# Optimization experiments

Hardware: AMD Instinct MI355X
Metric: run time of the kernel (lower is better)

## Reference

```python
import jax, jax.numpy as jnp
import numpy as np

B = 65536      # batch
D = 512        # embedding_dim
H = 256        # hidden_size
NB = 6         # num_branch


def setup_inputs() -> dict:
    key = jax.random.key(0)
    ks = jax.random.split(key, 12)
    sc = 0.05
    s = lambda k, shape: (jax.random.normal(k, shape, jnp.float32) * sc)
    inp = {}
    inp["embedding"] = jax.random.normal(ks[0], (B, D), jnp.float32)
    inp["speed"] = jax.random.normal(ks[1], (B,), jnp.float32)
    inp["command"] = jax.random.randint(ks[2], (B,), 1, NB + 1)  # values 1..6
    # speed_in: Linear(1,H) -> ReLU -> Linear(H,D)   (weights stored [in,out])
    inp["sw1"] = s(ks[3], (1, H)); inp["sb1"] = jnp.zeros((H,), jnp.float32)
    inp["sw2"] = s(ks[4], (H, D)); inp["sb2"] = jnp.zeros((D,), jnp.float32)
    # 6 branch MLPs, stacked along leading axis: D->H->H->3, sigmoid
    inp["bw1"] = s(ks[5], (NB, D, H)); inp["bb1"] = jnp.zeros((NB, H), jnp.float32)
    inp["bw2"] = s(ks[6], (NB, H, H)); inp["bb2"] = jnp.zeros((NB, H), jnp.float32)
    inp["bw3"] = s(ks[7], (NB, H, 3)); inp["bb3"] = jnp.zeros((NB, 3), jnp.float32)
    # speed_out: D->H->H->1
    inp["ow1"] = s(ks[8], (D, H)); inp["ob1"] = jnp.zeros((H,), jnp.float32)
    inp["ow2"] = s(ks[9], (H, H)); inp["ob2"] = jnp.zeros((H,), jnp.float32)
    inp["ow3"] = s(ks[10], (H, 1)); inp["ob3"] = jnp.zeros((1,), jnp.float32)
    return inp


def reference(embedding, speed, command,
              sw1, sb1, sw2, sb2,
              bw1, bb1, bw2, bb2, bw3, bb3,
              ow1, ob1, ow2, ob2, ow3, ob3):
    # embedding += speed_in(speed.unsqueeze(1))
    sh = jax.nn.relu(speed[:, None] @ sw1 + sb1)           # [B,H]
    emb = embedding + (sh @ sw2 + sb2)                      # [B,D]

    # all 6 branches computed densely (as in the original), then masked
    h = jax.nn.relu(jnp.einsum('bd,ndh->nbh', emb, bw1) + bb1[:, None, :])   # [NB,B,H]
    h = jax.nn.relu(jnp.einsum('nbh,nhk->nbk', h, bw2) + bb2[:, None, :])    # [NB,B,H]
    br = jax.nn.sigmoid(jnp.einsum('nbh,nho->nbo', h, bw3) + bb3[:, None, :])  # [NB,B,3]

    # mask: branch i selected where i == command - 1
    mask = (jnp.arange(NB)[:, None] == (command - 1)[None, :]).astype(br.dtype)  # [NB,B]
    control_pred = jnp.sum(br * mask[:, :, None], axis=0)   # [B,3]

    # speed_out head
    t = jax.nn.relu(emb @ ow1 + ob1)
    t = jax.nn.relu(t @ ow2 + ob2)
    speed_pred = t @ ow3 + ob3                               # [B,1]
    return control_pred, speed_pred
```

## Files before the change

kernel.cpp:

```cpp
#include <hip/hip_runtime.h>
#include <math.h>


#define B_ 65536
#define D_ 512
#define H_ 256

typedef float  f32x4   __attribute__((ext_vector_type(4)));
typedef __bf16 bf16x8  __attribute__((ext_vector_type(8)));
typedef __bf16 bf16x4  __attribute__((ext_vector_type(4)));
typedef float  float4v __attribute__((ext_vector_type(4)));

#define OFF_CURSORS  64
#define OFF_PERM     256
#define OFF_PACK     262400
#define WS_NEEDED    3277056

#define PKO_SW2   0u
#define PKO_BW1   131072u
#define PKO_BW2   917504u
#define PKO_OW1   1310720u
#define PKO_OW2   1441792u

#define PITCH_E 520
#define PITCH_H 264


__global__ __launch_bounds__(1024) void k_countscan(const int* __restrict__ command,
                                                    int* __restrict__ cursors) {
    __shared__ int red[6][1024];
    int t = threadIdx.x;
    int c0 = 0, c1 = 0, c2 = 0, c3 = 0, c4 = 0, c5 = 0;
    for (int i = t; i < B_; i += 1024) {
        int c = command[i] - 1; c = min(max(c, 0), 5);
        c0 += (c == 0); c1 += (c == 1); c2 += (c == 2);
        c3 += (c == 3); c4 += (c == 4); c5 += (c == 5);
    }
    red[0][t] = c0; red[1][t] = c1; red[2][t] = c2;
    red[3][t] = c3; red[4][t] = c4; red[5][t] = c5;
    __syncthreads();
    for (int s = 512; s > 0; s >>= 1) {
        if (t < s) {
            #pragma unroll
            for (int c = 0; c < 6; ++c) red[c][t] += red[c][t + s];
        }
        __syncthreads();
    }
    if (t == 0) {
        int sum = 0;
        #pragma unroll
        for (int c = 0; c < 6; ++c) { cursors[c] = sum; sum += red[c][0]; }
    }
}


__global__ __launch_bounds__(256) void k_prepB(const int* __restrict__ command,
                                               int* __restrict__ cursors,
                                               int* __restrict__ perm,
                                               const float* __restrict__ sw2,
                                               const float* __restrict__ bw1,
                                               const float* __restrict__ bw2,
                                               const float* __restrict__ ow1,
                                               const float* __restrict__ ow2,
                                               __bf16* __restrict__ PK) {
    int t = threadIdx.x;
    if (blockIdx.x < 256) {
        __shared__ int lh[6], lbase[6];
        if (t < 6) lh[t] = 0;
        __syncthreads();
        int i = blockIdx.x * 256 + t;
        int c = command[i] - 1; c = min(max(c, 0), 5);
        int rank = atomicAdd(&lh[c], 1);
        __syncthreads();
        if (t < 6) lbase[t] = atomicAdd(&cursors[t], lh[t]);
        __syncthreads();
        perm[lbase[c] + rank] = i;
        return;
    }
    int b = blockIdx.x - 256;
    const float* src; int srcN, colOff; unsigned dstOff; int tt;
    if (b < 64)       { int s = b >> 5;        tt = b & 31;  src = sw2;                          srcN = 512; colOff = s * 256; dstOff = PKO_SW2 + s * 65536u; }
    else if (b < 448) { int i = b - 64;  int c = i >> 6; tt = i & 63; src = bw1 + (size_t)c * 512 * 256; srcN = 256; colOff = 0; dstOff = PKO_BW1 + c * 131072u; }
    else if (b < 640) { int i = b - 448; int c = i >> 5; tt = i & 31; src = bw2 + (size_t)c * 256 * 256; srcN = 256; colOff = 0; dstOff = PKO_BW2 + c * 65536u; }
    else if (b < 704) { tt = b - 640; src = ow1; srcN = 256; colOff = 0; dstOff = PKO_OW1; }
    else              { tt = b - 704; src = ow2; srcN = 256; colOff = 0; dstOff = PKO_OW2; }
    int kc = tt >> 2, nt = tt & 3;
    int k0 = kc * 32, n0 = nt * 64;

    __shared__ __bf16 T[64][34];
    #pragma unroll
    for (int p = 0; p < 8; ++p) {
        int idx = p * 256 + t;
        int k = idx >> 6, n = idx & 63;
        T[n][k] = (__bf16)src[(size_t)(k0 + k) * srcN + colOff + n0 + n];
    }
    __syncthreads();
    int n = t >> 2, seg = t & 3;
    bf16x8 v;
    #pragma unroll
    for (int j = 0; j < 8; ++j) v[j] = T[n][seg * 8 + j];
    *(bf16x8*)(PK + dstOff + ((unsigned)(kc * 256 + n0 + n) * 32u + seg * 8u)) = v;
}


__global__ __launch_bounds__(256, 3) void k_fused(
    const float* __restrict__ embedding, const float* __restrict__ speed,
    const int*   __restrict__ command,
    const float* __restrict__ sw1, const float* __restrict__ sb1,
    const float* __restrict__ sb2,
    const float* __restrict__ bb1, const float* __restrict__ bb2,
    const float* __restrict__ bw3, const float* __restrict__ bb3,
    const float* __restrict__ ob1, const float* __restrict__ ob2,
    const float* __restrict__ ow3, const float* __restrict__ ob3,
    const int* __restrict__ perm, const __bf16* __restrict__ PK,
    float* __restrict__ out)
{
    __shared__ __bf16 s_emb[32 * PITCH_E];
    __shared__ __bf16 s_h[32 * PITCH_H];
    __shared__ float  s_head[32][4];
    __shared__ int    s_row[32];
    __shared__ int    s_cmd[32];
    __shared__ float  s_spd[32];

    const int tid = threadIdx.x;
    const int w = tid >> 6, lane = tid & 63;
    const int lm = lane & 15, kg = lane >> 4;
    const int R0 = blockIdx.x * 32;

    if (tid < 32) {
        int r = perm[R0 + tid];
        s_row[tid] = r;
        int c = command[r] - 1; c = min(max(c, 0), 5);
        s_cmd[tid] = c;
        s_spd[tid] = speed[r];
        s_head[tid][0] = 0.f; s_head[tid][1] = 0.f; s_head[tid][2] = 0.f; s_head[tid][3] = 0.f;
    }
    __syncthreads();

    #pragma unroll
    for (int it = 0; it < 16; ++it) {
        int idx = it * 256 + tid;
        int row = idx >> 7, c4 = idx & 127;
        float4v v = *(const float4v*)(embedding + (size_t)s_row[row] * D_ + c4 * 4);
        bf16x4 pv;
        pv[0] = (__bf16)v[0]; pv[1] = (__bf16)v[1];
        pv[2] = (__bf16)v[2]; pv[3] = (__bf16)v[3];
        *(bf16x4*)(s_emb + row * PITCH_E + c4 * 4) = pv;
    }
    __syncthreads();

    int cc[2][4];
    #pragma unroll
    for (int mt = 0; mt < 2; ++mt)
        #pragma unroll
        for (int g = 0; g < 4; ++g)
            cc[mt][g] = s_cmd[mt * 16 + kg * 4 + g];

    int myc = s_cmd[lane & 31];
    int cmin = myc, cmax = myc;
    #pragma unroll
    for (int d = 1; d < 32; d <<= 1) {
        cmin = min(cmin, __shfl_xor(cmin, d));
        cmax = max(cmax, __shfl_xor(cmax, d));
    }

    {
        const float spd0 = s_spd[lm], spd1 = s_spd[16 + lm];
        const unsigned slice = (unsigned)(w >> 1) * 65536u;
        const int mbase = (w & 1) * 128;
        f32x4 dacc[8][2];
        #pragma unroll
        for (int mt = 0; mt < 8; ++mt) {
            dacc[mt][0] = f32x4{0.f, 0.f, 0.f, 0.f};
            dacc[mt][1] = f32x4{0.f, 0.f, 0.f, 0.f};
        }
        #pragma unroll 2
        for (int ks = 0; ks < 8; ++ks) {
            const int k0 = ks * 32 + kg * 8;
            float4v w0 = *(const float4v*)(sw1 + k0);
            float4v w1 = *(const float4v*)(sw1 + k0 + 4);
            float4v c0 = *(const float4v*)(sb1 + k0);
            float4v c1 = *(const float4v*)(sb1 + k0 + 4);
            bf16x8 b0, b1;
            #pragma unroll
            for (int j = 0; j < 4; ++j) {
                b0[j]     = (__bf16)fmaxf(spd0 * w0[j] + c0[j], 0.f);
                b0[j + 4] = (__bf16)fmaxf(spd0 * w1[j] + c1[j], 0.f);
                b1[j]     = (__bf16)fmaxf(spd1 * w0[j] + c0[j], 0.f);
                b1[j + 4] = (__bf16)fmaxf(spd1 * w1[j] + c1[j], 0.f);
            }
            const __bf16* ap = PK + PKO_SW2 + slice + (size_t)ks * 8192
                             + (size_t)(mbase + lm) * 32 + kg * 8;
            #pragma unroll
            for (int mt = 0; mt < 8; ++mt) {
                bf16x8 av = *(const bf16x8*)(ap + mt * 512);
                dacc[mt][0] = __builtin_amdgcn_mfma_f32_16x16x32_bf16(av, b0, dacc[mt][0], 0, 0, 0);
                dacc[mt][1] = __builtin_amdgcn_mfma_f32_16x16x32_bf16(av, b1, dacc[mt][1], 0, 0, 0);
            }
        }
        #pragma unroll
        for (int mt = 0; mt < 8; ++mt) {
            int colb = w * 128 + mt * 16 + kg * 4;
            float4v sbv = *(const float4v*)(sb2 + colb);
            #pragma unroll
            for (int nt = 0; nt < 2; ++nt) {
                int row = nt * 16 + lm;
                bf16x4* p = (bf16x4*)(s_emb + row * PITCH_E + colb);
                bf16x4 old = *p;
                bf16x4 nv;
                #pragma unroll
                for (int g = 0; g < 4; ++g)
                    nv[g] = (__bf16)(dacc[mt][nt][g] + sbv[g] + (float)old[g]);
                *p = nv;
            }
        }
    }
    __syncthreads();

    const __bf16* aE0 = s_emb + lm * PITCH_E + kg * 8;
    const __bf16* aE1 = aE0 + 16 * PITCH_E;
    const __bf16* aH0 = s_h + lm * PITCH_H + kg * 8;
    const __bf16* aH1 = aH0 + 16 * PITCH_H;
    const size_t bcol = (size_t)(w * 64 + lm) * 32 + kg * 8;

    for (int c = cmin; c <= cmax; ++c) {
        f32x4 ah[2][4];
        #pragma unroll
        for (int mt = 0; mt < 2; ++mt)
            #pragma unroll
            for (int ct = 0; ct < 4; ++ct) ah[mt][ct] = f32x4{0.f, 0.f, 0.f, 0.f};
        const __bf16* bp = PK + PKO_BW1 + c * 131072u + bcol;
        #pragma unroll 2
        for (int ks = 0; ks < 16; ++ks) {
            bf16x8 a0 = *(const bf16x8*)(aE0 + ks * 32);
            bf16x8 a1 = *(const bf16x8*)(aE1 + ks * 32);
            #pragma unroll
            for (int ct = 0; ct < 4; ++ct) {
                bf16x8 bv = *(const bf16x8*)(bp + (size_t)ks * 8192 + ct * 512);
                ah[0][ct] = __builtin_amdgcn_mfma_f32_16x16x32_bf16(a0, bv, ah[0][ct], 0, 0, 0);
                ah[1][ct] = __builtin_amdgcn_mfma_f32_16x16x32_bf16(a1, bv, ah[1][ct], 0, 0, 0);
            }
        }
        #pragma unroll
        for (int ct = 0; ct < 4; ++ct) {
            int col = w * 64 + ct * 16 + lm;
            float b = bb1[c * H_ + col];
            #pragma unroll
            for (int mt = 0; mt < 2; ++mt)
                #pragma unroll
                for (int g = 0; g < 4; ++g)
                    if (cc[mt][g] == c) {
                        int row = mt * 16 + kg * 4 + g;
                        s_h[row * PITCH_H + col] = (__bf16)fmaxf(ah[mt][ct][g] + b, 0.f);
                    }
        }
    }
    __syncthreads();

    for (int c = cmin; c <= cmax; ++c) {
        f32x4 hh[2][4];
        #pragma unroll
        for (int mt = 0; mt < 2; ++mt)
            #pragma unroll
            for (int ct = 0; ct < 4; ++ct) hh[mt][ct] = f32x4{0.f, 0.f, 0.f, 0.f};
        const __bf16* bp = PK + PKO_BW2 + c * 65536u + bcol;
        #pragma unroll 2
        for (int ks = 0; ks < 8; ++ks) {
            bf16x8 a0 = *(const bf16x8*)(aH0 + ks * 32);
            bf16x8 a1 = *(const bf16x8*)(aH1 + ks * 32);
            #pragma unroll
            for (int ct = 0; ct < 4; ++ct) {
                bf16x8 bv = *(const bf16x8*)(bp + (size_t)ks * 8192 + ct * 512);
                hh[0][ct] = __builtin_amdgcn_mfma_f32_16x16x32_bf16(a0, bv, hh[0][ct], 0, 0, 0);
                hh[1][ct] = __builtin_amdgcn_mfma_f32_16x16x32_bf16(a1, bv, hh[1][ct], 0, 0, 0);
            }
        }
        float ph[2][4][3];
        #pragma unroll
        for (int mt = 0; mt < 2; ++mt)
            #pragma unroll
            for (int g = 0; g < 4; ++g) { ph[mt][g][0] = 0.f; ph[mt][g][1] = 0.f; ph[mt][g][2] = 0.f; }
        #pragma unroll
        for (int ct = 0; ct < 4; ++ct) {
            int col = w * 64 + ct * 16 + lm;
            float b  = bb2[c * H_ + col];
            float w0 = bw3[(c * H_ + col) * 3 + 0];
            float w1 = bw3[(c * H_ + col) * 3 + 1];
            float w2 = bw3[(c * H_ + col) * 3 + 2];
            #pragma unroll
            for (int mt = 0; mt < 2; ++mt)
                #pragma unroll
                for (int g = 0; g < 4; ++g) {
                    float h = fmaxf(hh[mt][ct][g] + b, 0.f);
                    ph[mt][g][0] += h * w0; ph[mt][g][1] += h * w1; ph[mt][g][2] += h * w2;
                }
        }
        #pragma unroll
        for (int mt = 0; mt < 2; ++mt)
            #pragma unroll
            for (int g = 0; g < 4; ++g)
                #pragma unroll
                for (int o = 0; o < 3; ++o) {
                    float v = ph[mt][g][o];
                    v += __shfl_xor(v, 1); v += __shfl_xor(v, 2);
                    v += __shfl_xor(v, 4); v += __shfl_xor(v, 8);
                    ph[mt][g][o] = v;
                }
        if (lm == 0) {
            #pragma unroll
            for (int mt = 0; mt < 2; ++mt)
                #pragma unroll
                for (int g = 0; g < 4; ++g)
                    if (cc[mt][g] == c) {
                        int row = mt * 16 + kg * 4 + g;
                        atomicAdd(&s_head[row][0], ph[mt][g][0]);
                        atomicAdd(&s_head[row][1], ph[mt][g][1]);
                        atomicAdd(&s_head[row][2], ph[mt][g][2]);
                    }
        }
    }
    __syncthreads();

    {
        f32x4 ta[2][4];
        #pragma unroll
        for (int mt = 0; mt < 2; ++mt)
            #pragma unroll
            for (int ct = 0; ct < 4; ++ct) ta[mt][ct] = f32x4{0.f, 0.f, 0.f, 0.f};
        const __bf16* bp = PK + PKO_OW1 + bcol;
        #pragma unroll 2
        for (int ks = 0; ks < 16; ++ks) {
            bf16x8 a0 = *(const bf16x8*)(aE0 + ks * 32);
            bf16x8 a1 = *(const bf16x8*)(aE1 + ks * 32);
            #pragma unroll
            for (int ct = 0; ct < 4; ++ct) {
                bf16x8 bv = *(const bf16x8*)(bp + (size_t)ks * 8192 + ct * 512);
                ta[0][ct] = __builtin_amdgcn_mfma_f32_16x16x32_bf16(a0, bv, ta[0][ct], 0, 0, 0);
                ta[1][ct] = __builtin_amdgcn_mfma_f32_16x16x32_bf16(a1, bv, ta[1][ct], 0, 0, 0);
            }
        }
        #pragma unroll
        for (int ct = 0; ct < 4; ++ct) {
            int col = w * 64 + ct * 16 + lm;
            float b = ob1[col];
            #pragma unroll
            for (int mt = 0; mt < 2; ++mt)
                #pragma unroll
                for (int g = 0; g < 4; ++g) {
                    int row = mt * 16 + kg * 4 + g;
                    s_h[row * PITCH_H + col] = (__bf16)fmaxf(ta[mt][ct][g] + b, 0.f);
                }
        }
    }
    __syncthreads();

    {
        f32x4 sa[2][4];
        #pragma unroll
        for (int mt = 0; mt < 2; ++mt)
            #pragma unroll
            for (int ct = 0; ct < 4; ++ct) sa[mt][ct] = f32x4{0.f, 0.f, 0.f, 0.f};
        const __bf16* bp = PK + PKO_OW2 + bcol;
        #pragma unroll 2
        for (int ks = 0; ks < 8; ++ks) {
            bf16x8 a0 = *(const bf16x8*)(aH0 + ks * 32);
            bf16x8 a1 = *(const bf16x8*)(aH1 + ks * 32);
            #pragma unroll
            for (int ct = 0; ct < 4; ++ct) {
                bf16x8 bv = *(const bf16x8*)(bp + (size_t)ks * 8192 + ct * 512);
                sa[0][ct] = __builtin_amdgcn_mfma_f32_16x16x32_bf16(a0, bv, sa[0][ct], 0, 0, 0);
                sa[1][ct] = __builtin_amdgcn_mfma_f32_16x16x32_bf16(a1, bv, sa[1][ct], 0, 0, 0);
            }
        }
        float sp[2][4];
        #pragma unroll
        for (int mt = 0; mt < 2; ++mt)
            #pragma unroll
            for (int g = 0; g < 4; ++g) sp[mt][g] = 0.f;
        #pragma unroll
        for (int ct = 0; ct < 4; ++ct) {
            int col = w * 64 + ct * 16 + lm;
            float b = ob2[col], wv = ow3[col];
            #pragma unroll
            for (int mt = 0; mt < 2; ++mt)
                #pragma unroll
                for (int g = 0; g < 4; ++g)
                    sp[mt][g] += fmaxf(sa[mt][ct][g] + b, 0.f) * wv;
        }
        #pragma unroll
        for (int mt = 0; mt < 2; ++mt)
            #pragma unroll
            for (int g = 0; g < 4; ++g) {
                float v = sp[mt][g];
                v += __shfl_xor(v, 1); v += __shfl_xor(v, 2);
                v += __shfl_xor(v, 4); v += __shfl_xor(v, 8);
                if (lm == 0) atomicAdd(&s_head[mt * 16 + kg * 4 + g][3], v);
            }
    }
    __syncthreads();

    if (tid < 32) {
        int r = s_row[tid], c = s_cmd[tid];
        #pragma unroll
        for (int o = 0; o < 3; ++o) {
            float x = s_head[tid][o] + bb3[c * 3 + o];
            out[(size_t)r * 3 + o] = 1.f / (1.f + __expf(-x));
        }
        out[(size_t)3 * B_ + r] = s_head[tid][3] + ob3[0];
    }
}


__global__ __launch_bounds__(256) void cilrs_slow(
    const float* __restrict__ embedding, const float* __restrict__ speed,
    const int* __restrict__ command,
    const float* __restrict__ sw1, const float* __restrict__ sb1,
    const float* __restrict__ sw2, const float* __restrict__ sb2,
    const float* __restrict__ bw1, const float* __restrict__ bb1,
    const float* __restrict__ bw2, const float* __restrict__ bb2,
    const float* __restrict__ bw3, const float* __restrict__ bb3,
    const float* __restrict__ ow1, const float* __restrict__ ob1,
    const float* __restrict__ ow2, const float* __restrict__ ob2,
    const float* __restrict__ ow3, const float* __restrict__ ob3,
    float* __restrict__ out)
{
    const int row = blockIdx.x;
    const int j   = threadIdx.x;
    __shared__ float sh[H_];
    __shared__ float emb[D_];
    __shared__ float h1[H_];
    __shared__ float h2[H_];
    const float spd = speed[row];
    { float v = spd * sw1[j] + sb1[j]; sh[j] = v > 0.f ? v : 0.f; }
    __syncthreads();
    {
        float a0 = 0.f, a1 = 0.f;
        for (int h = 0; h < H_; ++h) {
            const float s = sh[h];
            a0 += s * sw2[h * D_ + j];
            a1 += s * sw2[h * D_ + j + 256];
        }
        emb[j]       = embedding[(size_t)row * D_ + j]       + a0 + sb2[j];
        emb[j + 256] = embedding[(size_t)row * D_ + j + 256] + a1 + sb2[j + 256];
    }
    __syncthreads();
    const int n = command[row] - 1;
    {
        const float* wp = bw1 + (size_t)n * D_ * H_;
        float a = 0.f;
        for (int d = 0; d < D_; ++d) a += emb[d] * wp[d * H_ + j];
        a += bb1[n * H_ + j];
        h1[j] = a > 0.f ? a : 0.f;
    }
    __syncthreads();
    {
        const float* wp = bw2 + (size_t)n * H_ * H_;
        float a = 0.f;
        for (int h = 0; h < H_; ++h) a += h1[h] * wp[h * H_ + j];
        a += bb2[n * H_ + j];
        h2[j] = a > 0.f ? a : 0.f;
    }
    __syncthreads();
    {
        float a = 0.f;
        for (int d = 0; d < D_; ++d) a += emb[d] * ow1[d * H_ + j];
        a += ob1[j];
        sh[j] = a > 0.f ? a : 0.f;
    }
    __syncthreads();
    {
        float a = 0.f;
        for (int h = 0; h < H_; ++h) a += sh[h] * ow2[h * H_ + j];
        a += ob2[j];
        h1[j] = a > 0.f ? a : 0.f;
    }
    __syncthreads();
    if (j < 3) {
        const float* wp = bw3 + (size_t)n * H_ * 3;
        float a = 0.f;
        for (int h = 0; h < H_; ++h) a += h2[h] * wp[h * 3 + j];
        a += bb3[n * 3 + j];
        out[(size_t)row * 3 + j] = 1.f / (1.f + expf(-a));
    } else if (j == 3) {
        float a = 0.f;
        for (int h = 0; h < H_; ++h) a += h1[h] * ow3[h];
        a += ob3[0];
        out[(size_t)B_ * 3 + row] = a;
    }
}


extern "C" void kernel_launch(void* const* d_in, const int* in_sizes, int n_in,
                              void* d_out, int out_size, void* d_ws, size_t ws_size,
                              hipStream_t stream) {
    const float* embedding = (const float*)d_in[0];
    const float* speed     = (const float*)d_in[1];
    const int*   command   = (const int*)  d_in[2];
    const float* sw1 = (const float*)d_in[3];
    const float* sb1 = (const float*)d_in[4];
    const float* sw2 = (const float*)d_in[5];
    const float* sb2 = (const float*)d_in[6];
    const float* bw1 = (const float*)d_in[7];
    const float* bb1 = (const float*)d_in[8];
    const float* bw2 = (const float*)d_in[9];
    const float* bb2 = (const float*)d_in[10];
    const float* bw3 = (const float*)d_in[11];
    const float* bb3 = (const float*)d_in[12];
    const float* ow1 = (const float*)d_in[13];
    const float* ob1 = (const float*)d_in[14];
    const float* ow2 = (const float*)d_in[15];
    const float* ob2 = (const float*)d_in[16];
    const float* ow3 = (const float*)d_in[17];
    const float* ob3 = (const float*)d_in[18];
    float* out = (float*)d_out;

    if (ws_size < (size_t)WS_NEEDED) {
        cilrs_slow<<<B_, 256, 0, stream>>>(embedding, speed, command,
                                           sw1, sb1, sw2, sb2,
                                           bw1, bb1, bw2, bb2, bw3, bb3,
                                           ow1, ob1, ow2, ob2, ow3, ob3, out);
        return;
    }

    char* ws = (char*)d_ws;
    int*    cursors = (int*)   (ws + OFF_CURSORS);
    int*    perm    = (int*)   (ws + OFF_PERM);
    __bf16* PK      = (__bf16*)(ws + OFF_PACK);

    k_countscan<<<1, 1024, 0, stream>>>(command, cursors);
    k_prepB<<<992, 256, 0, stream>>>(command, cursors, perm,
                                     sw2, bw1, bw2, ow1, ow2, PK);
    k_fused<<<B_ / 32, 256, 0, stream>>>(embedding, speed, command,
                                         sw1, sb1, sb2,
                                         bb1, bb2, bw3, bb3,
                                         ob1, ob2, ow3, ob3,
                                         perm, PK, out);
}
```

Measured before the change: 390.9 us.

## Split warps between branch and speed heads, drop separate hidden buffer

The four-phase sequential schedule (branch L1, branch L2, speed L1, speed L2), in which all four warps took part in each phase, is replaced by a split. Warps 0-1 run the branch MLP and warps 2-3 run the speed head concurrently, each warp covering 128 columns in two halves. Layer-1 results are held in registers and then written back into the reused embedding LDS buffer, so the separate s_h array goes away. That lowers LDS use and lets launch bounds rise to 4 blocks per CU. The change also adds vectorized int4 command counting and nontemporal loads and stores, at the cost of higher per-warp register pressure and a possible imbalance when a block spans several commands.

After: 415.2 us. +6.2%, slower.

```diff
diff --git a/kernel.cpp b/kernel.cpp
--- a/kernel.cpp
+++ b/kernel.cpp
@@ -23,21 +23,26 @@
 #define PKO_OW2   1441792u
 
 #define PITCH_E 520
-#define PITCH_H 264
 
 
 __global__ __launch_bounds__(1024) void k_countscan(const int* __restrict__ command,
                                                     int* __restrict__ cursors) {
     __shared__ int red[6][1024];
     int t = threadIdx.x;
-    int c0 = 0, c1 = 0, c2 = 0, c3 = 0, c4 = 0, c5 = 0;
-    for (int i = t; i < B_; i += 1024) {
-        int c = command[i] - 1; c = min(max(c, 0), 5);
-        c0 += (c == 0); c1 += (c == 1); c2 += (c == 2);
-        c3 += (c == 3); c4 += (c == 4); c5 += (c == 5);
-    }
-    red[0][t] = c0; red[1][t] = c1; red[2][t] = c2;
-    red[3][t] = c3; red[4][t] = c4; red[5][t] = c5;
+    int cnt[6] = {0, 0, 0, 0, 0, 0};
+    const int4* c4p = (const int4*)command;
+    for (int i = t; i < B_ / 4; i += 1024) {
+        int4 v = c4p[i];
+        int a[4] = {v.x, v.y, v.z, v.w};
+        #pragma unroll
+        for (int j = 0; j < 4; ++j) {
+            int c = min(max(a[j] - 1, 0), 5);
+            #pragma unroll
+            for (int k = 0; k < 6; ++k) cnt[k] += (c == k);
+        }
+    }
+    #pragma unroll
+    for (int k = 0; k < 6; ++k) red[k][t] = cnt[k];
     __syncthreads();
     for (int s = 512; s > 0; s >>= 1) {
         if (t < s) {
@@ -103,7 +108,7 @@
 }
 
 
-__global__ __launch_bounds__(256, 3) void k_fused(
+__global__ __launch_bounds__(256, 4) void k_fused(
     const float* __restrict__ embedding, const float* __restrict__ speed,
     const int*   __restrict__ command,
     const float* __restrict__ sw1, const float* __restrict__ sb1,
@@ -115,8 +120,7 @@
     const int* __restrict__ perm, const __bf16* __restrict__ PK,
     float* __restrict__ out)
 {
-    __shared__ __bf16 s_emb[32 * PITCH_E];
-    __shared__ __bf16 s_h[32 * PITCH_H];
+    __shared__ __bf16 s_x[32 * PITCH_E];
     __shared__ float  s_head[32][4];
     __shared__ int    s_row[32];
     __shared__ int    s_cmd[32];
@@ -141,11 +145,12 @@
     for (int it = 0; it < 16; ++it) {
         int idx = it * 256 + tid;
         int row = idx >> 7, c4 = idx & 127;
-        float4v v = *(const float4v*)(embedding + (size_t)s_row[row] * D_ + c4 * 4);
+        float4v v = __builtin_nontemporal_load(
+            (const float4v*)(embedding + (size_t)s_row[row] * D_ + c4 * 4));
         bf16x4 pv;
         pv[0] = (__bf16)v[0]; pv[1] = (__bf16)v[1];
         pv[2] = (__bf16)v[2]; pv[3] = (__bf16)v[3];
-        *(bf16x4*)(s_emb + row * PITCH_E + c4 * 4) = pv;
+        *(bf16x4*)(s_x + row * PITCH_E + c4 * 4) = pv;
     }
     __syncthreads();
 
@@ -205,7 +210,7 @@
             #pragma unroll
             for (int nt = 0; nt < 2; ++nt) {
                 int row = nt * 16 + lm;
-                bf16x4* p = (bf16x4*)(s_emb + row * PITCH_E + colb);
+                bf16x4* p = (bf16x4*)(s_x + row * PITCH_E + colb);
                 bf16x4 old = *p;
                 bf16x4 nv;
                 #pragma unroll
@@ -217,175 +222,202 @@
     }
     __syncthreads();
 
-    const __bf16* aE0 = s_emb + lm * PITCH_E + kg * 8;
-    const __bf16* aE1 = aE0 + 16 * PITCH_E;
-    const __bf16* aH0 = s_h + lm * PITCH_H + kg * 8;
-    const __bf16* aH1 = aH0 + 16 * PITCH_H;
-    const size_t bcol = (size_t)(w * 64 + lm) * 32 + kg * 8;
-
-    for (int c = cmin; c <= cmax; ++c) {
-        f32x4 ah[2][4];
+    const int wq = w & 1;
+    const bool roleB = (w < 2);
+    const __bf16* aX0 = s_x + lm * PITCH_E + kg * 8;
+    const __bf16* aX1 = aX0 + 16 * PITCH_E;
+    const unsigned laneoff = (unsigned)(wq * 128 + lm) * 32u + kg * 8u;
+
+    bf16x4 res[2][8];
+    if (roleB) {
+        for (int c = cmin; c <= cmax; ++c) {
+            const __bf16* bb = PK + PKO_BW1 + c * 131072u + laneoff;
+            #pragma unroll
+            for (int half = 0; half < 2; ++half) {
+                f32x4 ah[2][4];
+                #pragma unroll
+                for (int mt = 0; mt < 2; ++mt)
+                    #pragma unroll
+                    for (int ct = 0; ct < 4; ++ct) ah[mt][ct] = f32x4{0.f, 0.f, 0.f, 0.f};
+                const __bf16* bp = bb + half * 2048;
+                #pragma unroll 2
+                for (int ks = 0; ks < 16; ++ks) {
+                    bf16x8 a0 = *(const bf16x8*)(aX0 + ks * 32);
+                    bf16x8 a1 = *(const bf16x8*)(aX1 + ks * 32);
+                    #pragma unroll
+                    for (int ct = 0; ct < 4; ++ct) {
+                        bf16x8 bv = *(const bf16x8*)(bp + (size_t)ks * 8192 + ct * 512);
+                        ah[0][ct] = __builtin_amdgcn_mfma_f32_16x16x32_bf16(a0, bv, ah[0][ct], 0, 0, 0);
+                        ah[1][ct] = __builtin_amdgcn_mfma_f32_16x16x32_bf16(a1, bv, ah[1][ct], 0, 0, 0);
+                    }
+                }
+                #pragma unroll
+                for (int ct = 0; ct < 4; ++ct) {
+                    int col = wq * 128 + (half * 4 + ct) * 16 + lm;
+                    float b = bb1[c * H_ + col];
+                    #pragma unroll
+                    for (int mt = 0; mt < 2; ++mt)
+                        #pragma unroll
+                        for (int g = 0; g < 4; ++g)
+                            if (cc[mt][g] == c)
+                                res[mt][half * 4 + ct][g] = (__bf16)fmaxf(ah[mt][ct][g] + b, 0.f);
+                }
+            }
+        }
+    } else {
+        const __bf16* bb = PK + PKO_OW1 + laneoff;
+        #pragma unroll
+        for (int half = 0; half < 2; ++half) {
+            f32x4 ta[2][4];
+            #pragma unroll
+            for (int mt = 0; mt < 2; ++mt)
+                #pragma unroll
+                for (int ct = 0; ct < 4; ++ct) ta[mt][ct] = f32x4{0.f, 0.f, 0.f, 0.f};
+            const __bf16* bp = bb + half * 2048;
+            #pragma unroll 2
+            for (int ks = 0; ks < 16; ++ks) {
+                bf16x8 a0 = *(const bf16x8*)(aX0 + ks * 32);
+                bf16x8 a1 = *(const bf16x8*)(aX1 + ks * 32);
+                #pragma unroll
+                for (int ct = 0; ct < 4; ++ct) {
+                    bf16x8 bv = *(const bf16x8*)(bp + (size_t)ks * 8192 + ct * 512);
+                    ta[0][ct] = __builtin_amdgcn_mfma_f32_16x16x32_bf16(a0, bv, ta[0][ct], 0, 0, 0);
+                    ta[1][ct] = __builtin_amdgcn_mfma_f32_16x16x32_bf16(a1, bv, ta[1][ct], 0, 0, 0);
+                }
+            }
+            #pragma unroll
+            for (int ct = 0; ct < 4; ++ct) {
+                int col = wq * 128 + (half * 4 + ct) * 16 + lm;
+                float b = ob1[col];
+                #pragma unroll
+                for (int mt = 0; mt < 2; ++mt)
+                    #pragma unroll
+                    for (int g = 0; g < 4; ++g)
+                        res[mt][half * 4 + ct][g] = (__bf16)fmaxf(ta[mt][ct][g] + b, 0.f);
+            }
+        }
+    }
+    __syncthreads();
+
+    {
+        const int colBase = (roleB ? 0 : 256) + wq * 128;
+        #pragma unroll
+        for (int ct = 0; ct < 8; ++ct) {
+            int col = colBase + ct * 16 + lm;
+            #pragma unroll
+            for (int mt = 0; mt < 2; ++mt)
+                #pragma unroll
+                for (int g = 0; g < 4; ++g)
+                    s_x[(mt * 16 + kg * 4 + g) * PITCH_E + col] = res[mt][ct][g];
+        }
+    }
+    __syncthreads();
+
+    const __bf16* aH0 = s_x + lm * PITCH_E + (roleB ? 0 : 256) + kg * 8;
+    const __bf16* aH1 = aH0 + 16 * PITCH_E;
+    if (roleB) {
+        for (int c = cmin; c <= cmax; ++c) {
+            float ph[2][4][3];
+            #pragma unroll
+            for (int mt = 0; mt < 2; ++mt)
+                #pragma unroll
+                for (int g = 0; g < 4; ++g) { ph[mt][g][0] = 0.f; ph[mt][g][1] = 0.f; ph[mt][g][2] = 0.f; }
+            const __bf16* bb = PK + PKO_BW2 + c * 65536u + laneoff;
+            #pragma unroll
+            for (int half = 0; half < 2; ++half) {
+                f32x4 hh[2][4];
+                #pragma unroll
+                for (int mt = 0; mt < 2; ++mt)
+                    #pragma unroll
+                    for (int ct = 0; ct < 4; ++ct) hh[mt][ct] = f32x4{0.f, 0.f, 0.f, 0.f};
+                const __bf16* bp = bb + half * 2048;
+                #pragma unroll 2
+                for (int ks = 0; ks < 8; ++ks) {
+                    bf16x8 a0 = *(const bf16x8*)(aH0 + ks * 32);
+                    bf16x8 a1 = *(const bf16x8*)(aH1 + ks * 32);
+                    #pragma unroll
+                    for (int ct = 0; ct < 4; ++ct) {
+                        bf16x8 bv = *(const bf16x8*)(bp + (size_t)ks * 8192 + ct * 512);
+                        hh[0][ct] = __builtin_amdgcn_mfma_f32_16x16x32_bf16(a0, bv, hh[0][ct], 0, 0, 0);
+                        hh[1][ct] = __builtin_amdgcn_mfma_f32_16x16x32_bf16(a1, bv, hh[1][ct], 0, 0, 0);
+                    }
+                }
+                #pragma unroll
+                for (int ct = 0; ct < 4; ++ct) {
+                    int col = wq * 128 + (half * 4 + ct) * 16 + lm;
+                    float b  = bb2[c * H_ + col];
+                    float w0 = bw3[(c * H_ + col) * 3 + 0];
+                    float w1 = bw3[(c * H_ + col) * 3 + 1];
+                    float w2 = bw3[(c * H_ + col) * 3 + 2];
+                    #pragma unroll
+                    for (int mt = 0; mt < 2; ++mt)
+                        #pragma unroll
+                        for (int g = 0; g < 4; ++g) {
+                            float h = fmaxf(hh[mt][ct][g] + b, 0.f);
+                            ph[mt][g][0] += h * w0; ph[mt][g][1] += h * w1; ph[mt][g][2] += h * w2;
+                        }
+                }
+            }
+            #pragma unroll
+            for (int mt = 0; mt < 2; ++mt)
+                #pragma unroll
+                for (int g = 0; g < 4; ++g)
+                    #pragma unroll
+                    for (int o = 0; o < 3; ++o) {
+                        float v = ph[mt][g][o];
+                        v += __shfl_xor(v, 1); v += __shfl_xor(v, 2);
+                        v += __shfl_xor(v, 4); v += __shfl_xor(v, 8);
+                        ph[mt][g][o] = v;
+                    }
+            if (lm == 0) {
+                #pragma unroll
+                for (int mt = 0; mt < 2; ++mt)
+                    #pragma unroll
+                    for (int g = 0; g < 4; ++g)
+                        if (cc[mt][g] == c) {
+                            int row = mt * 16 + kg * 4 + g;
+                            atomicAdd(&s_head[row][0], ph[mt][g][0]);
+                            atomicAdd(&s_head[row][1], ph[mt][g][1]);
+                            atomicAdd(&s_head[row][2], ph[mt][g][2]);
+                        }
+            }
+        }
+    } else {
+        float sp[2][4];
         #pragma unroll
         for (int mt = 0; mt < 2; ++mt)
             #pragma unroll
-            for (int ct = 0; ct < 4; ++ct) ah[mt][ct] = f32x4{0.f, 0.f, 0.f, 0.f};
-        const __bf16* bp = PK + PKO_BW1 + c * 131072u + bcol;
-        #pragma unroll 2
-        for (int ks = 0; ks < 16; ++ks) {
-            bf16x8 a0 = *(const bf16x8*)(aE0 + ks * 32);
-            bf16x8 a1 = *(const bf16x8*)(aE1 + ks * 32);
+            for (int g = 0; g < 4; ++g) sp[mt][g] = 0.f;
+        const __bf16* bb = PK + PKO_OW2 + laneoff;
+        #pragma unroll
+        for (int half = 0; half < 2; ++half) {
+            f32x4 hh[2][4];
+            #pragma unroll
+            for (int mt = 0; mt < 2; ++mt)
+                #pragma unroll
+                for (int ct = 0; ct < 4; ++ct) hh[mt][ct] = f32x4{0.f, 0.f, 0.f, 0.f};
+            const __bf16* bp = bb + half * 2048;
+            #pragma unroll 2
+            for (int ks = 0; ks < 8; ++ks) {
+                bf16x8 a0 = *(const bf16x8*)(aH0 + ks * 32);
+                bf16x8 a1 = *(const bf16x8*)(aH1 + ks * 32);
+                #pragma unroll
+                for (int ct = 0; ct < 4; ++ct) {
+                    bf16x8 bv = *(const bf16x8*)(bp + (size_t)ks * 8192 + ct * 512);
+                    hh[0][ct] = __builtin_amdgcn_mfma_f32_16x16x32_bf16(a0, bv, hh[0][ct], 0, 0, 0);
+                    hh[1][ct] = __builtin_amdgcn_mfma_f32_16x16x32_bf16(a1, bv, hh[1][ct], 0, 0, 0);
+                }
+            }
             #pragma unroll
             for (int ct = 0; ct < 4; ++ct) {
-                bf16x8 bv = *(const bf16x8*)(bp + (size_t)ks * 8192 + ct * 512);
-                ah[0][ct] = __builtin_amdgcn_mfma_f32_16x16x32_bf16(a0, bv, ah[0][ct], 0, 0, 0);
-                ah[1][ct] = __builtin_amdgcn_mfma_f32_16x16x32_bf16(a1, bv, ah[1][ct], 0, 0, 0);
-            }
-        }
-        #pragma unroll
-        for (int ct = 0; ct < 4; ++ct) {
-            int col = w * 64 + ct * 16 + lm;
-            float b = bb1[c * H_ + col];
-            #pragma unroll
-            for (int mt = 0; mt < 2; ++mt)
-                #pragma unroll
-                for (int g = 0; g < 4; ++g)
-                    if (cc[mt][g] == c) {
-                        int row = mt * 16 + kg * 4 + g;
-                        s_h[row * PITCH_H + col] = (__bf16)fmaxf(ah[mt][ct][g] + b, 0.f);
-                    }
-        }
-    }
-    __syncthreads();
-
-    for (int c = cmin; c <= cmax; ++c) {
-        f32x4 hh[2][4];
-        #pragma unroll
-        for (int mt = 0; mt < 2; ++mt)
-            #pragma unroll
-            for (int ct = 0; ct < 4; ++ct) hh[mt][ct] = f32x4{0.f, 0.f, 0.f, 0.f};
-        const __bf16* bp = PK + PKO_BW2 + c * 65536u + bcol;
-        #pragma unroll 2
-        for (int ks = 0; ks < 8; ++ks) {
-            bf16x8 a0 = *(const bf16x8*)(aH0 + ks * 32);
-            bf16x8 a1 = *(const bf16x8*)(aH1 + ks * 32);
-            #pragma unroll
-            for (int ct = 0; ct < 4; ++ct) {
-                bf16x8 bv = *(const bf16x8*)(bp + (size_t)ks * 8192 + ct * 512);
-                hh[0][ct] = __builtin_amdgcn_mfma_f32_16x16x32_bf16(a0, bv, hh[0][ct], 0, 0, 0);
-                hh[1][ct] = __builtin_amdgcn_mfma_f32_16x16x32_bf16(a1, bv, hh[1][ct], 0, 0, 0);
-            }
-        }
-        float ph[2][4][3];
-        #pragma unroll
-        for (int mt = 0; mt < 2; ++mt)
-            #pragma unroll
-            for (int g = 0; g < 4; ++g) { ph[mt][g][0] = 0.f; ph[mt][g][1] = 0.f; ph[mt][g][2] = 0.f; }
-        #pragma unroll
-        for (int ct = 0; ct < 4; ++ct) {
-            int col = w * 64 + ct * 16 + lm;
-            float b  = bb2[c * H_ + col];
-            float w0 = bw3[(c * H_ + col) * 3 + 0];
-            float w1 = bw3[(c * H_ + col) * 3 + 1];
-            float w2 = bw3[(c * H_ + col) * 3 + 2];
-            #pragma unroll
-            for (int mt = 0; mt < 2; ++mt)
-                #pragma unroll
-                for (int g = 0; g < 4; ++g) {
-                    float h = fmaxf(hh[mt][ct][g] + b, 0.f);
-                    ph[mt][g][0] += h * w0; ph[mt][g][1] += h * w1; ph[mt][g][2] += h * w2;
-                }
-        }
-        #pragma unroll
-        for (int mt = 0; mt < 2; ++mt)
-            #pragma unroll
-            for (int g = 0; g < 4; ++g)
-                #pragma unroll
-                for (int o = 0; o < 3; ++o) {
-                    float v = ph[mt][g][o];
-                    v += __shfl_xor(v, 1); v += __shfl_xor(v, 2);
-                    v += __shfl_xor(v, 4); v += __shfl_xor(v, 8);
-                    ph[mt][g][o] = v;
-                }
-        if (lm == 0) {
-            #pragma unroll
-            for (int mt = 0; mt < 2; ++mt)
-                #pragma unroll
-                for (int g = 0; g < 4; ++g)
-                    if (cc[mt][g] == c) {
-                        int row = mt * 16 + kg * 4 + g;
-                        atomicAdd(&s_head[row][0], ph[mt][g][0]);
-                        atomicAdd(&s_head[row][1], ph[mt][g][1]);
-                        atomicAdd(&s_head[row][2], ph[mt][g][2]);
-                    }
-        }
-    }
-    __syncthreads();
-
-    {
-        f32x4 ta[2][4];
-        #pragma unroll
-        for (int mt = 0; mt < 2; ++mt)
-            #pragma unroll
-            for (int ct = 0; ct < 4; ++ct) ta[mt][ct] = f32x4{0.f, 0.f, 0.f, 0.f};
-        const __bf16* bp = PK + PKO_OW1 + bcol;
-        #pragma unroll 2
-        for (int ks = 0; ks < 16; ++ks) {
-            bf16x8 a0 = *(const bf16x8*)(aE0 + ks * 32);
-            bf16x8 a1 = *(const bf16x8*)(aE1 + ks * 32);
-            #pragma unroll
-            for (int ct = 0; ct < 4; ++ct) {
-                bf16x8 bv = *(const bf16x8*)(bp + (size_t)ks * 8192 + ct * 512);
-                ta[0][ct] = __builtin_amdgcn_mfma_f32_16x16x32_bf16(a0, bv, ta[0][ct], 0, 0, 0);
-                ta[1][ct] = __builtin_amdgcn_mfma_f32_16x16x32_bf16(a1, bv, ta[1][ct], 0, 0, 0);
-            }
-        }
-        #pragma unroll
-        for (int ct = 0; ct < 4; ++ct) {
-            int col = w * 64 + ct * 16 + lm;
-            float b = ob1[col];
-            #pragma unroll
-            for (int mt = 0; mt < 2; ++mt)
-                #pragma unroll
-                for (int g = 0; g < 4; ++g) {
-                    int row = mt * 16 + kg * 4 + g;
-                    s_h[row * PITCH_H + col] = (__bf16)fmaxf(ta[mt][ct][g] + b, 0.f);
-                }
-        }
-    }
-    __syncthreads();
-
-    {
-        f32x4 sa[2][4];
-        #pragma unroll
-        for (int mt = 0; mt < 2; ++mt)
-            #pragma unroll
-            for (int ct = 0; ct < 4; ++ct) sa[mt][ct] = f32x4{0.f, 0.f, 0.f, 0.f};
-        const __bf16* bp = PK + PKO_OW2 + bcol;
-        #pragma unroll 2
-        for (int ks = 0; ks < 8; ++ks) {
-            bf16x8 a0 = *(const bf16x8*)(aH0 + ks * 32);
-            bf16x8 a1 = *(const bf16x8*)(aH1 + ks * 32);
-            #pragma unroll
-            for (int ct = 0; ct < 4; ++ct) {
-                bf16x8 bv = *(const bf16x8*)(bp + (size_t)ks * 8192 + ct * 512);
-                sa[0][ct] = __builtin_amdgcn_mfma_f32_16x16x32_bf16(a0, bv, sa[0][ct], 0, 0, 0);
-                sa[1][ct] = __builtin_amdgcn_mfma_f32_16x16x32_bf16(a1, bv, sa[1][ct], 0, 0, 0);
-            }
-        }
-        float sp[2][4];
-        #pragma unroll
-        for (int mt = 0; mt < 2; ++mt)
-            #pragma unroll
-            for (int g = 0; g < 4; ++g) sp[mt][g] = 0.f;
-        #pragma unroll
-        for (int ct = 0; ct < 4; ++ct) {
-            int col = w * 64 + ct * 16 + lm;
-            float b = ob2[col], wv = ow3[col];
-            #pragma unroll
-            for (int mt = 0; mt < 2; ++mt)
-                #pragma unroll
-                for (int g = 0; g < 4; ++g)
-                    sp[mt][g] += fmaxf(sa[mt][ct][g] + b, 0.f) * wv;
+                int col = wq * 128 + (half * 4 + ct) * 16 + lm;
+                float b = ob2[col], wv = ow3[col];
+                #pragma unroll
+                for (int mt = 0; mt < 2; ++mt)
+                    #pragma unroll
+                    for (int g = 0; g < 4; ++g)
+                        sp[mt][g] += fmaxf(hh[mt][ct][g] + b, 0.f) * wv;
+            }
         }
         #pragma unroll
         for (int mt = 0; mt < 2; ++mt)
@@ -404,9 +436,9 @@
         #pragma unroll
         for (int o = 0; o < 3; ++o) {
             float x = s_head[tid][o] + bb3[c * 3 + o];
-            out[(size_t)r * 3 + o] = 1.f / (1.f + __expf(-x));
-        }
-        out[(size_t)3 * B_ + r] = s_head[tid][3] + ob3[0];
+            __builtin_nontemporal_store(1.f / (1.f + __expf(-x)), &out[(size_t)r * 3 + o]);
+        }
+        __builtin_nontemporal_store(s_head[tid][3] + ob3[0], &out[(size_t)3 * B_ + r]);
     }
 }
 
```
